# Optimization experiments

Hardware: AMD Instinct MI355X
Metric: run time of the kernel (lower is better)

## Reference

```python
import jax, jax.numpy as jnp
import numpy as np
import math

V, H, NH, L, S, B = 100000, 2048, 64, 2, 512, 2
HD = H // NH  # 32
MAX_LEN = 5000
EPS_NORM = 1e-5
EPS_ATTN = 1e-6


def build_pe():
    # PositionalEncoding buffer: pe[max_len, 1, d_model]
    position = jnp.arange(MAX_LEN, dtype=jnp.float32)[:, None]
    div_term = jnp.exp(jnp.arange(0, H, 2, dtype=jnp.float32) * (-math.log(10000.0) / H))
    ang = position * div_term  # [max_len, H/2]
    pe = jnp.zeros((MAX_LEN, 1, H), dtype=jnp.float32)
    pe = pe.at[:, 0, 0::2].set(jnp.sin(ang))
    pe = pe.at[:, 0, 1::2].set(jnp.cos(ang))
    return pe


def fast_inv_sqrt(x):
    # Quake fast inverse sqrt; the bit-trick seed is detached in the original
    x2 = x * 0.5
    i = jax.lax.bitcast_convert_type(jax.lax.stop_gradient(x.astype(jnp.float32)), jnp.int32)
    i = jnp.int32(1597463007) - (i >> 1)
    y = jax.lax.bitcast_convert_type(i, jnp.float32)
    return y * (1.5 - x2 * y * y)  # grad flows only through x2, as in torch


def sr_norm(h, w, b):
    mean = h.mean(-1, keepdims=True)
    var = ((h - mean) ** 2).mean(-1, keepdims=True)  # biased variance
    inv = fast_inv_sqrt(var + EPS_NORM)
    return w * ((h - mean) * inv) + b


def attn_layer(x, wq, bq, wk, bk, wv, bv, wo, bo, nw, nb):
    # x: [B, S, H]; weights stored [in, out]
    def heads(t):
        return t.reshape(B, S, NH, HD).transpose(0, 2, 1, 3)  # [B, NH, S, HD]
    q = heads(x @ wq + bq)
    k = heads(x @ wk + bk)
    v = heads(x @ wv + bv)
    scores = jnp.einsum('bhqd,bhkd->bhqk', q, k) / math.sqrt(HD)
    a = jax.nn.softmax(scores, axis=-1)
    # dropout is identity in eval; then double softmax (exp/sum) + sigmoid gate
    e = jnp.exp(a)
    a2 = e / (e.sum(-1, keepdims=True) + EPS_ATTN)
    cw = a2 * jax.nn.sigmoid(a2)
    o = jnp.einsum('bhqk,bhkd->bhqd', cw, v)
    o = o.transpose(0, 2, 1, 3).reshape(B, S, H)
    o = o @ wo + bo
    return sr_norm(o + x, nw, nb)


def setup_inputs():
    key = jax.random.key(0)
    ks = jax.random.split(key, 12)
    def rn(k, shape):
        return jax.random.normal(k, shape, dtype=jnp.float32) * 0.02
    return {
        'src': jax.random.randint(ks[0], (B, S), 0, V),
        'emb': jax.random.uniform(ks[1], (V, H), minval=-0.1, maxval=0.1, dtype=jnp.float32),
        'Wq': rn(ks[2], (L, H, H)), 'bq': jnp.zeros((L, H), jnp.float32),
        'Wk': rn(ks[3], (L, H, H)), 'bk': jnp.zeros((L, H), jnp.float32),
        'Wv': rn(ks[4], (L, H, H)), 'bv': jnp.zeros((L, H), jnp.float32),
        'Wo': rn(ks[5], (L, H, H)), 'bo': jnp.zeros((L, H), jnp.float32),
        'nw': jnp.ones((L, H), jnp.float32), 'nb': jnp.zeros((L, H), jnp.float32),
        'Wout': jax.random.uniform(ks[6], (H, V), minval=-0.1, maxval=0.1, dtype=jnp.float32),
        'bout': jnp.zeros((V,), jnp.float32),
    }


def reference(src, emb, Wq, bq, Wk, bk, Wv, bv, Wo, bo, nw, nb, Wout, bout):
    x = emb[src] * math.sqrt(H)  # [B, S, H]
    pe = build_pe()
    # Faithful to pe[:x.size(0)] where x is [B, S, H]: indexes by BATCH dim
    x = x + pe[:x.shape[0]]  # [B, 1, H] broadcast over seq
    for l in range(L):
        x = attn_layer(x, Wq[l], bq[l], Wk[l], bk[l], Wv[l], bv[l],
                       Wo[l], bo[l], nw[l], nb[l])
    return x @ Wout + bout  # [B, S, V]
```

## Files before the change

kernel.cpp:

```cpp
#include <hip/hip_runtime.h>


#define DEVINL __device__ __forceinline__

typedef float f32x4 __attribute__((ext_vector_type(4)));
typedef __bf16 bf16x8 __attribute__((ext_vector_type(8)));

DEVINL unsigned short f2bf(float f) {
  unsigned int u = __float_as_uint(f);
  u += 0x7fffu + ((u >> 16) & 1u);
  return (unsigned short)(u >> 16);
}

DEVINL void gload_lds16(const void* g, void* l) {
  __builtin_amdgcn_global_load_lds(
      (const __attribute__((address_space(1))) unsigned int*)g,
      (__attribute__((address_space(3))) unsigned int*)l, 16, 0, 0);
}

__global__ __launch_bounds__(256) void embed_kernel(
    const int* __restrict__ src, const float* __restrict__ emb,
    float* __restrict__ x, unsigned short* __restrict__ xbf) {
  const int row = blockIdx.x;
  const int b = row >> 9;
  const int tok = src[row];
  const float sqrtH = 45.25483399593904f;
  const float c = -9.210340371976184f / 2048.f;
  for (int h = threadIdx.x; h < 2048; h += 256) {
    int i = h >> 1;
    float dv = expf((float)(2 * i) * c);
    float ang = (float)b * dv;
    float pe = (h & 1) ? cosf(ang) : sinf(ang);
    float val = emb[(size_t)tok * 2048 + h] * sqrtH + pe;
    x[(size_t)row * 2048 + h] = val;
    xbf[(size_t)row * 2048 + h] = f2bf(val);
  }
}

template <int BM>
DEVINL void gemm_body(const unsigned short* __restrict__ A, const float* __restrict__ B,
                      const float* __restrict__ bias, float* __restrict__ C,
                      const int N, const int m0, const int n0) {
  constexpr int K = 2048;
  constexpr int WM = BM / 32;
  constexpr int AI = BM / 64;
  __shared__ __align__(16) unsigned short A_lds[2][BM * 32];
  __shared__ __align__(16) unsigned short B_lds[2][128 * 32];

  const int tid = threadIdx.x;
  const int w = tid >> 6, lane = tid & 63;
  const int wm = w >> 1, wn = w & 1;

  const int n_local = tid & 127;
  const int kq = tid >> 7;
  const int col = n0 + n_local;
  const bool colok = col < N;
  const int bswz = (n_local >> 1) & 3;

  const int aRow = lane >> 2;
  const int aChunk = (lane & 3) ^ ((lane >> 3) & 3);

  int aOff[WM], bOff[4];
#pragma unroll
  for (int mi = 0; mi < WM; ++mi) {
    int m = wm * (BM / 2) + mi * 16 + (lane & 15);
    aOff[mi] = m * 32 + ((lane >> 4) ^ ((m >> 1) & 3)) * 8;
  }
#pragma unroll
  for (int ni = 0; ni < 4; ++ni) {
    int n = wn * 64 + ni * 16 + (lane & 15);
    bOff[ni] = n * 32 + ((lane >> 4) ^ ((n >> 1) & 3)) * 8;
  }

  f32x4 acc[WM][4] = {};
  float fB[16];

  auto stageA = [&](int k0, int bf) {
#pragma unroll
    for (int i = 0; i < AI; ++i) {
      int r0 = (w * AI + i) * 16;
      gload_lds16(A + (size_t)(m0 + r0 + aRow) * K + k0 + aChunk * 8,
                  &A_lds[bf][r0 * 32]);
    }
  };
  auto loadB = [&](int k0) {
#pragma unroll
    for (int g = 0; g < 4; ++g) {
      int kl = (g * 2 + kq) * 4;
#pragma unroll
      for (int i = 0; i < 4; ++i)
        fB[g * 4 + i] = colok ? B[(size_t)(k0 + kl + i) * N + col] : 0.f;
    }
  };
  auto writeB = [&](int bf) {
#pragma unroll
    for (int g = 0; g < 4; ++g) {
      int kl = (g * 2 + kq) * 4;
      unsigned int lo = (unsigned int)f2bf(fB[g * 4 + 0]) | ((unsigned int)f2bf(fB[g * 4 + 1]) << 16);
      unsigned int hi = (unsigned int)f2bf(fB[g * 4 + 2]) | ((unsigned int)f2bf(fB[g * 4 + 3]) << 16);
      int chunk = (kl >> 3) ^ bswz;
      *(uint2*)&B_lds[bf][n_local * 32 + chunk * 8 + (kl & 7)] = make_uint2(lo, hi);
    }
  };
  auto compute = [&](int bf) {
    bf16x8 af[WM], bfr[4];
#pragma unroll
    for (int mi = 0; mi < WM; ++mi) af[mi] = *(const bf16x8*)&A_lds[bf][aOff[mi]];
#pragma unroll
    for (int ni = 0; ni < 4; ++ni) bfr[ni] = *(const bf16x8*)&B_lds[bf][bOff[ni]];
#pragma unroll
    for (int mi = 0; mi < WM; ++mi)
#pragma unroll
      for (int ni = 0; ni < 4; ++ni)
        acc[mi][ni] = __builtin_amdgcn_mfma_f32_16x16x32_bf16(af[mi], bfr[ni], acc[mi][ni], 0, 0, 0);
  };

  stageA(0, 0);
  loadB(0);
  writeB(0);
  __syncthreads();
  int buf = 0;
  for (int t = 0; t < K / 32 - 1; ++t) {
    stageA((t + 1) * 32, buf ^ 1);
    loadB((t + 1) * 32);
    compute(buf);
    writeB(buf ^ 1);
    __syncthreads();
    buf ^= 1;
  }
  compute(buf);

  const int r0w = (lane >> 4) * 4;
  const int lrow = lane & 15;
#pragma unroll
  for (int mi = 0; mi < WM; ++mi)
#pragma unroll
    for (int ni = 0; ni < 4; ++ni) {
      int ccol = n0 + wn * 64 + ni * 16 + lrow;
      if (ccol < N) {
        float bv = bias[ccol];
#pragma unroll
        for (int r = 0; r < 4; ++r) {
          int crow = m0 + wm * (BM / 2) + mi * 16 + r0w + r;
          C[(size_t)crow * N + ccol] = acc[mi][ni][r] + bv;
        }
      }
    }
}

template <int BM>
__global__ __launch_bounds__(256) void gemm_kernel(
    const unsigned short* __restrict__ A, const float* __restrict__ B,
    const float* __restrict__ bias, float* __restrict__ C, const int N) {
  gemm_body<BM>(A, B, bias, C, N, blockIdx.x * BM, blockIdx.y * 128);
}

__global__ __launch_bounds__(256) void gemm_qkv_kernel(
    const unsigned short* __restrict__ A,
    const float* __restrict__ Wq, const float* __restrict__ Wk, const float* __restrict__ Wv,
    const float* __restrict__ bq, const float* __restrict__ bk, const float* __restrict__ bv,
    float* __restrict__ q, float* __restrict__ k, float* __restrict__ v) {
  const int z = blockIdx.z;
  const float* B = (z == 0) ? Wq : (z == 1) ? Wk : Wv;
  const float* bias = (z == 0) ? bq : (z == 1) ? bk : bv;
  float* C = (z == 0) ? q : (z == 1) ? k : v;
  gemm_body<64>(A, B, bias, C, 2048, blockIdx.x * 64, blockIdx.y * 128);
}

__global__ __launch_bounds__(256) void gemm_final_kernel(
    const unsigned short* __restrict__ A, const float* __restrict__ B,
    const float* __restrict__ bias, float* __restrict__ C, const int N) {
  const int bid = blockIdx.x;
  const int f = (bid & 7) * (gridDim.x >> 3) + (bid >> 3);
  gemm_body<128>(A, B, bias, C, N, (f & 7) * 128, (f >> 3) * 128);
}

__global__ __launch_bounds__(256) void attn_kernel(
    const float* __restrict__ q, const float* __restrict__ k,
    const float* __restrict__ v, unsigned short* __restrict__ o) {
  __shared__ __align__(16) float K_lds[512 * 32];
  const int tid = threadIdx.x;
  const int blk = blockIdx.x;
  const int bh = blk >> 1, chunk = blk & 1;
  const int b = bh >> 6, h = bh & 63;
  const size_t headoff = (size_t)b * 512 * 2048 + (size_t)h * 32;

  const float* kb = k + headoff;
#pragma unroll
  for (int i = 0; i < 16; ++i) {
    int flat = i * 256 + tid;
    int j = flat >> 3, d4 = flat & 7;
    *(float4*)&K_lds[j * 32 + d4 * 4] = *(const float4*)(kb + (size_t)j * 2048 + d4 * 4);
  }
  __syncthreads();

  const int row = chunk * 256 + tid;
  const float* qr = q + headoff + (size_t)row * 2048;
  float4 Q[8];
#pragma unroll
  for (int d = 0; d < 8; ++d) Q[d] = *(const float4*)(qr + d * 4);

  const float scale = 0.17677669529663689f;
  auto dot = [&](int j) -> float {
    const float4* kr = (const float4*)&K_lds[j * 32];
    float p0 = 0.f, p1 = 0.f, p2 = 0.f, p3 = 0.f;
#pragma unroll
    for (int d = 0; d < 8; ++d) {
      float4 kk = kr[d];
      p0 = fmaf(Q[d].x, kk.x, p0);
      p1 = fmaf(Q[d].y, kk.y, p1);
      p2 = fmaf(Q[d].z, kk.z, p2);
      p3 = fmaf(Q[d].w, kk.w, p3);
    }
    return ((p0 + p1) + (p2 + p3)) * scale;
  };

  float m = -1e30f, denom = 0.f;
  for (int j = 0; j < 512; ++j) {
    float s = dot(j);
    float nm = fmaxf(m, s);
    denom = denom * __expf(m - nm) + __expf(s - nm);
    m = nm;
  }
  const float invd = 1.f / denom;

  float sum_e = 0.f;
  for (int j = 0; j < 512; ++j) {
    float a = __expf(dot(j) - m) * invd;
    sum_e += __expf(a);
  }
  const float inv_se = 1.f / (sum_e + 1e-6f);

  float4 accv[8];
#pragma unroll
  for (int d = 0; d < 8; ++d) accv[d] = make_float4(0.f, 0.f, 0.f, 0.f);
  const float* vb = v + headoff;
  float4 vcur[8];
#pragma unroll
  for (int d = 0; d < 8; ++d) vcur[d] = ((const float4*)vb)[d];
  for (int j = 0; j < 512; ++j) {
    float4 vnxt[8];
    if (j < 511) {
      const float4* vr = (const float4*)(vb + (size_t)(j + 1) * 2048);
#pragma unroll
      for (int d = 0; d < 8; ++d) vnxt[d] = vr[d];
    } else {
#pragma unroll
      for (int d = 0; d < 8; ++d) vnxt[d] = vcur[d];
    }
    float a = __expf(dot(j) - m) * invd;
    float e = __expf(a);
    float a2 = e * inv_se;
    float cw = a2 / (1.f + __expf(-a2));
#pragma unroll
    for (int d = 0; d < 8; ++d) {
      accv[d].x = fmaf(cw, vcur[d].x, accv[d].x);
      accv[d].y = fmaf(cw, vcur[d].y, accv[d].y);
      accv[d].z = fmaf(cw, vcur[d].z, accv[d].z);
      accv[d].w = fmaf(cw, vcur[d].w, accv[d].w);
    }
#pragma unroll
    for (int d = 0; d < 8; ++d) vcur[d] = vnxt[d];
  }
  unsigned short* orow = o + headoff + (size_t)row * 2048;
#pragma unroll
  for (int d = 0; d < 8; ++d) {
    orow[d * 4 + 0] = f2bf(accv[d].x);
    orow[d * 4 + 1] = f2bf(accv[d].y);
    orow[d * 4 + 2] = f2bf(accv[d].z);
    orow[d * 4 + 3] = f2bf(accv[d].w);
  }
}

__global__ __launch_bounds__(256) void norm_kernel(
    const float* __restrict__ o, const float* __restrict__ xin,
    const float* __restrict__ w, const float* __restrict__ bb,
    float* __restrict__ xout, unsigned short* __restrict__ xbf) {
  __shared__ float red[4];
  const int row = blockIdx.x, tid = threadIdx.x;
  const float* op = o + (size_t)row * 2048;
  const float* xp = xin + (size_t)row * 2048;
  float4 hv[2];
#pragma unroll
  for (int i = 0; i < 2; ++i) {
    float4 a = *(const float4*)(op + tid * 4 + i * 1024);
    float4 c = *(const float4*)(xp + tid * 4 + i * 1024);
    hv[i] = make_float4(a.x + c.x, a.y + c.y, a.z + c.z, a.w + c.w);
  }
  float s = 0.f;
#pragma unroll
  for (int i = 0; i < 2; ++i) s += hv[i].x + hv[i].y + hv[i].z + hv[i].w;
  for (int off = 32; off; off >>= 1) s += __shfl_down(s, off);
  if ((tid & 63) == 0) red[tid >> 6] = s;
  __syncthreads();
  const float mean = (red[0] + red[1] + red[2] + red[3]) * (1.f / 2048.f);
  __syncthreads();

  float vs = 0.f;
#pragma unroll
  for (int i = 0; i < 2; ++i) {
    float dx = hv[i].x - mean, dy = hv[i].y - mean, dz = hv[i].z - mean, dw = hv[i].w - mean;
    vs += dx * dx + dy * dy + dz * dz + dw * dw;
  }
  for (int off = 32; off; off >>= 1) vs += __shfl_down(vs, off);
  if ((tid & 63) == 0) red[tid >> 6] = vs;
  __syncthreads();
  const float var = (red[0] + red[1] + red[2] + red[3]) * (1.f / 2048.f);

  const float xv = var + 1e-5f;
  int ii = __float_as_int(xv);
  ii = 1597463007 - (ii >> 1);
  float y = __int_as_float(ii);
  y = y * (1.5f - 0.5f * xv * y * y);

#pragma unroll
  for (int i = 0; i < 2; ++i) {
    int c0 = tid * 4 + i * 1024;
    float4 wv = *(const float4*)(w + c0);
    float4 bv = *(const float4*)(bb + c0);
    float r0 = wv.x * ((hv[i].x - mean) * y) + bv.x;
    float r1 = wv.y * ((hv[i].y - mean) * y) + bv.y;
    float r2 = wv.z * ((hv[i].z - mean) * y) + bv.z;
    float r3 = wv.w * ((hv[i].w - mean) * y) + bv.w;
    *(float4*)(xout + (size_t)row * 2048 + c0) = make_float4(r0, r1, r2, r3);
    unsigned short* xb = xbf + (size_t)row * 2048 + c0;
    xb[0] = f2bf(r0); xb[1] = f2bf(r1); xb[2] = f2bf(r2); xb[3] = f2bf(r3);
  }
}

extern "C" void kernel_launch(void* const* d_in, const int* in_sizes, int n_in,
                              void* d_out, int out_size, void* d_ws, size_t ws_size,
                              hipStream_t stream) {
  const int*   src  = (const int*)d_in[0];
  const float* emb  = (const float*)d_in[1];
  const float* Wq   = (const float*)d_in[2];
  const float* bq   = (const float*)d_in[3];
  const float* Wk   = (const float*)d_in[4];
  const float* bk   = (const float*)d_in[5];
  const float* Wv   = (const float*)d_in[6];
  const float* bv   = (const float*)d_in[7];
  const float* Wo   = (const float*)d_in[8];
  const float* bo   = (const float*)d_in[9];
  const float* nw   = (const float*)d_in[10];
  const float* nb   = (const float*)d_in[11];
  const float* Wout = (const float*)d_in[12];
  const float* bout = (const float*)d_in[13];
  float* out = (float*)d_out;

  char* ws = (char*)d_ws;
  float* x  = (float*)(ws);
  float* qb = (float*)(ws + (8ll << 20));
  float* kb = (float*)(ws + (16ll << 20));
  float* vb = (float*)(ws + (24ll << 20));
  float* ob = (float*)(ws + (32ll << 20));
  unsigned short* xbf = (unsigned short*)(ws + (40ll << 20));
  unsigned short* abf = (unsigned short*)(ws + (44ll << 20));

  embed_kernel<<<1024, 256, 0, stream>>>(src, emb, x, xbf);

  for (int l = 0; l < 2; ++l) {
    const size_t wo_ = (size_t)l * 2048 * 2048;
    const size_t bo_ = (size_t)l * 2048;
    gemm_qkv_kernel<<<dim3(16, 16, 3), 256, 0, stream>>>(
        xbf, Wq + wo_, Wk + wo_, Wv + wo_, bq + bo_, bk + bo_, bv + bo_, qb, kb, vb);
    attn_kernel<<<256, 256, 0, stream>>>(qb, kb, vb, abf);
    gemm_kernel<64><<<dim3(16, 16), 256, 0, stream>>>(abf, Wo + wo_, bo + bo_, ob, 2048);
    norm_kernel<<<1024, 256, 0, stream>>>(ob, x, nw + bo_, nb + bo_, x, xbf);
  }

  gemm_final_kernel<<<8 * 782, 256, 0, stream>>>(xbf, Wout, bout, out, 100000);
}
```

Before: 2.095 ms.

## Pre-transpose weights to bf16 K-major and load GEMM B tiles directly to LDS

Adds a transpose kernel that converts each fp32 weight matrix into a bf16 [N,K] copy in workspace. GEMMs then stage B tiles with direct global-to-LDS loads instead of strided fp32 loads followed by in-register conversion. The conversion runs every call and rereads the full 800MB Wout while writing a 400MB bf16 copy, so it adds traffic in exchange for cheaper GEMM inner loops. Also switches bf16 packing to native conversions with vectorised stores. It falls back to the old path when the workspace is too small.

```diff
diff --git a/kernel.cpp b/kernel.cpp
--- a/kernel.cpp
+++ b/kernel.cpp
@@ -5,11 +5,18 @@
 
 typedef float f32x4 __attribute__((ext_vector_type(4)));
 typedef __bf16 bf16x8 __attribute__((ext_vector_type(8)));
-
-DEVINL unsigned short f2bf(float f) {
-  unsigned int u = __float_as_uint(f);
-  u += 0x7fffu + ((u >> 16) & 1u);
-  return (unsigned short)(u >> 16);
+typedef __bf16 bf16x2v __attribute__((ext_vector_type(2)));
+
+DEVINL unsigned int pk2(float a, float b) {
+  bf16x2v v;
+  v[0] = (__bf16)a;
+  v[1] = (__bf16)b;
+  return __builtin_bit_cast(unsigned int, v);
+}
+
+DEVINL unsigned short bf1(float a) {
+  __bf16 v = (__bf16)a;
+  return __builtin_bit_cast(unsigned short, v);
 }
 
 DEVINL void gload_lds16(const void* g, void* l) {
@@ -33,8 +40,140 @@
     float pe = (h & 1) ? cosf(ang) : sinf(ang);
     float val = emb[(size_t)tok * 2048 + h] * sqrtH + pe;
     x[(size_t)row * 2048 + h] = val;
-    xbf[(size_t)row * 2048 + h] = f2bf(val);
-  }
+    xbf[(size_t)row * 2048 + h] = bf1(val);
+  }
+}
+
+__global__ __launch_bounds__(256) void wtrans_kernel(
+    const float* __restrict__ W, unsigned short* __restrict__ WT, const int N) {
+  __shared__ float t[64][65];
+  const int tid = threadIdx.x;
+  const int n0 = blockIdx.x * 64, k0 = blockIdx.y * 64;
+#pragma unroll
+  for (int i = 0; i < 16; ++i) {
+    int kl = i * 4 + (tid >> 6);
+    int n = n0 + (tid & 63);
+    t[kl][tid & 63] = (n < N) ? W[(size_t)(k0 + kl) * N + n] : 0.f;
+  }
+  __syncthreads();
+#pragma unroll
+  for (int j = 0; j < 8; ++j) {
+    int nl = j * 8 + (tid >> 5);
+    int kp = (tid & 31) * 2;
+    unsigned int u = pk2(t[kp][nl], t[kp + 1][nl]);
+    *(unsigned int*)&WT[(size_t)(n0 + nl) * 2048 + k0 + kp] = u;
+  }
+}
+
+template <int BM, int NN>
+DEVINL void gemm_bf_body(const unsigned short* __restrict__ A,
+                         const unsigned short* __restrict__ BT,
+                         const float* __restrict__ bias, float* __restrict__ C,
+                         const int m0, const int n0) {
+  constexpr int K = 2048;
+  constexpr int WM = BM / 32;
+  __shared__ __align__(16) unsigned short A_lds[2][BM * 32];
+  __shared__ __align__(16) unsigned short B_lds[2][128 * 32];
+
+  const int tid = threadIdx.x;
+  const int w = tid >> 6, lane = tid & 63;
+  const int wm = w >> 1, wn = w & 1;
+
+  const int aRow = lane >> 2;
+  const int aChunk = (lane & 3) ^ ((lane >> 3) & 3);
+
+  int aOff[WM], bOff[4];
+#pragma unroll
+  for (int mi = 0; mi < WM; ++mi) {
+    int m = wm * (BM / 2) + mi * 16 + (lane & 15);
+    aOff[mi] = m * 32 + ((lane >> 4) ^ ((m >> 1) & 3)) * 8;
+  }
+#pragma unroll
+  for (int ni = 0; ni < 4; ++ni) {
+    int n = wn * 64 + ni * 16 + (lane & 15);
+    bOff[ni] = n * 32 + ((lane >> 4) ^ ((n >> 1) & 3)) * 8;
+  }
+
+  f32x4 acc[WM][4] = {};
+
+  auto stage = [&](int k0, int bf) {
+#pragma unroll
+    for (int i = 0; i < BM / 64; ++i) {
+      int r0 = (w * (BM / 64) + i) * 16;
+      gload_lds16(A + (size_t)(m0 + r0 + aRow) * K + k0 + aChunk * 8, &A_lds[bf][r0 * 32]);
+    }
+#pragma unroll
+    for (int i = 0; i < 2; ++i) {
+      int r0 = (w * 2 + i) * 16;
+      gload_lds16(BT + (size_t)(n0 + r0 + aRow) * K + k0 + aChunk * 8, &B_lds[bf][r0 * 32]);
+    }
+  };
+  auto compute = [&](int bf) {
+    bf16x8 af[WM], bfr[4];
+#pragma unroll
+    for (int mi = 0; mi < WM; ++mi) af[mi] = *(const bf16x8*)&A_lds[bf][aOff[mi]];
+#pragma unroll
+    for (int ni = 0; ni < 4; ++ni) bfr[ni] = *(const bf16x8*)&B_lds[bf][bOff[ni]];
+#pragma unroll
+    for (int mi = 0; mi < WM; ++mi)
+#pragma unroll
+      for (int ni = 0; ni < 4; ++ni)
+        acc[mi][ni] = __builtin_amdgcn_mfma_f32_16x16x32_bf16(af[mi], bfr[ni], acc[mi][ni], 0, 0, 0);
+  };
+
+  stage(0, 0);
+  __syncthreads();
+  int buf = 0;
+  for (int t = 0; t < K / 32 - 1; ++t) {
+    stage((t + 1) * 32, buf ^ 1);
+    compute(buf);
+    __syncthreads();
+    buf ^= 1;
+  }
+  compute(buf);
+
+  const int r0w = (lane >> 4) * 4;
+  const int lrow = lane & 15;
+#pragma unroll
+  for (int mi = 0; mi < WM; ++mi)
+#pragma unroll
+    for (int ni = 0; ni < 4; ++ni) {
+      int ccol = n0 + wn * 64 + ni * 16 + lrow;
+      if ((NN % 128 == 0) || ccol < NN) {
+        float bv = bias[ccol];
+#pragma unroll
+        for (int r = 0; r < 4; ++r) {
+          int crow = m0 + wm * (BM / 2) + mi * 16 + r0w + r;
+          C[(size_t)crow * NN + ccol] = acc[mi][ni][r] + bv;
+        }
+      }
+    }
+}
+
+template <int BM, int NN>
+__global__ __launch_bounds__(256) void gemm_bf_kernel(
+    const unsigned short* __restrict__ A, const unsigned short* __restrict__ BT,
+    const float* __restrict__ bias, float* __restrict__ C) {
+  gemm_bf_body<BM, NN>(A, BT, bias, C, blockIdx.x * BM, blockIdx.y * 128);
+}
+
+__global__ __launch_bounds__(256) void gemm_qkv_bf_kernel(
+    const unsigned short* __restrict__ A, const unsigned short* __restrict__ WT,
+    const float* __restrict__ bq, const float* __restrict__ bk, const float* __restrict__ bv,
+    float* __restrict__ q, float* __restrict__ k, float* __restrict__ v) {
+  const int z = blockIdx.z;
+  const unsigned short* BT = WT + (size_t)z * 2048 * 2048;
+  const float* bias = (z == 0) ? bq : (z == 1) ? bk : bv;
+  float* C = (z == 0) ? q : (z == 1) ? k : v;
+  gemm_bf_body<64, 2048>(A, BT, bias, C, blockIdx.x * 64, blockIdx.y * 128);
+}
+
+__global__ __launch_bounds__(256) void gemm_final_bf_kernel(
+    const unsigned short* __restrict__ A, const unsigned short* __restrict__ BT,
+    const float* __restrict__ bias, float* __restrict__ C) {
+  const int bid = blockIdx.x;
+  const int f = (bid & 7) * (gridDim.x >> 3) + (bid >> 3);
+  gemm_bf_body<128, 100000>(A, BT, bias, C, (f & 7) * 128, (f >> 3) * 128);
 }
 
 template <int BM>
@@ -79,8 +218,7 @@
 #pragma unroll
     for (int i = 0; i < AI; ++i) {
       int r0 = (w * AI + i) * 16;
-      gload_lds16(A + (size_t)(m0 + r0 + aRow) * K + k0 + aChunk * 8,
-                  &A_lds[bf][r0 * 32]);
+      gload_lds16(A + (size_t)(m0 + r0 + aRow) * K + k0 + aChunk * 8, &A_lds[bf][r0 * 32]);
     }
   };
   auto loadB = [&](int k0) {
@@ -96,10 +234,10 @@
 #pragma unroll
     for (int g = 0; g < 4; ++g) {
       int kl = (g * 2 + kq) * 4;
-      unsigned int lo = (unsigned int)f2bf(fB[g * 4 + 0]) | ((unsigned int)f2bf(fB[g * 4 + 1]) << 16);
-      unsigned int hi = (unsigned int)f2bf(fB[g * 4 + 2]) | ((unsigned int)f2bf(fB[g * 4 + 3]) << 16);
+      uint2 p = make_uint2(pk2(fB[g * 4 + 0], fB[g * 4 + 1]),
+                           pk2(fB[g * 4 + 2], fB[g * 4 + 3]));
       int chunk = (kl >> 3) ^ bswz;
-      *(uint2*)&B_lds[bf][n_local * 32 + chunk * 8 + (kl & 7)] = make_uint2(lo, hi);
+      *(uint2*)&B_lds[bf][n_local * 32 + chunk * 8 + (kl & 7)] = p;
     }
   };
   auto compute = [&](int bf) {
@@ -146,13 +284,6 @@
         }
       }
     }
-}
-
-template <int BM>
-__global__ __launch_bounds__(256) void gemm_kernel(
-    const unsigned short* __restrict__ A, const float* __restrict__ B,
-    const float* __restrict__ bias, float* __restrict__ C, const int N) {
-  gemm_body<BM>(A, B, bias, C, N, blockIdx.x * BM, blockIdx.y * 128);
 }
 
 __global__ __launch_bounds__(256) void gemm_qkv_kernel(
@@ -167,6 +298,13 @@
   gemm_body<64>(A, B, bias, C, 2048, blockIdx.x * 64, blockIdx.y * 128);
 }
 
+template <int BM>
+__global__ __launch_bounds__(256) void gemm_kernel(
+    const unsigned short* __restrict__ A, const float* __restrict__ B,
+    const float* __restrict__ bias, float* __restrict__ C, const int N) {
+  gemm_body<BM>(A, B, bias, C, N, blockIdx.x * BM, blockIdx.y * 128);
+}
+
 __global__ __launch_bounds__(256) void gemm_final_kernel(
     const unsigned short* __restrict__ A, const float* __restrict__ B,
     const float* __restrict__ bias, float* __restrict__ C, const int N) {
@@ -265,10 +403,8 @@
   unsigned short* orow = o + headoff + (size_t)row * 2048;
 #pragma unroll
   for (int d = 0; d < 8; ++d) {
-    orow[d * 4 + 0] = f2bf(accv[d].x);
-    orow[d * 4 + 1] = f2bf(accv[d].y);
-    orow[d * 4 + 2] = f2bf(accv[d].z);
-    orow[d * 4 + 3] = f2bf(accv[d].w);
+    uint2 p = make_uint2(pk2(accv[d].x, accv[d].y), pk2(accv[d].z, accv[d].w));
+    *(uint2*)&orow[d * 4] = p;
   }
 }
 
@@ -323,8 +459,7 @@
     float r2 = wv.z * ((hv[i].z - mean) * y) + bv.z;
     float r3 = wv.w * ((hv[i].w - mean) * y) + bv.w;
     *(float4*)(xout + (size_t)row * 2048 + c0) = make_float4(r0, r1, r2, r3);
-    unsigned short* xb = xbf + (size_t)row * 2048 + c0;
-    xb[0] = f2bf(r0); xb[1] = f2bf(r1); xb[2] = f2bf(r2); xb[3] = f2bf(r3);
+    *(uint2*)&xbf[(size_t)row * 2048 + c0] = make_uint2(pk2(r0, r1), pk2(r2, r3));
   }
 }
 
@@ -356,17 +491,44 @@
   unsigned short* xbf = (unsigned short*)(ws + (40ll << 20));
   unsigned short* abf = (unsigned short*)(ws + (44ll << 20));
 
+  const unsigned long long NEED = (112ull << 20) + 100096ull * 2048ull * 2ull;
+  const bool big = (unsigned long long)ws_size >= NEED;
+  unsigned short* WTp = (unsigned short*)(ws + (48ll << 20));
+  unsigned short* WTo = (unsigned short*)(ws + (112ll << 20));
+
   embed_kernel<<<1024, 256, 0, stream>>>(src, emb, x, xbf);
 
-  for (int l = 0; l < 2; ++l) {
-    const size_t wo_ = (size_t)l * 2048 * 2048;
-    const size_t bo_ = (size_t)l * 2048;
-    gemm_qkv_kernel<<<dim3(16, 16, 3), 256, 0, stream>>>(
-        xbf, Wq + wo_, Wk + wo_, Wv + wo_, bq + bo_, bk + bo_, bv + bo_, qb, kb, vb);
-    attn_kernel<<<256, 256, 0, stream>>>(qb, kb, vb, abf);
-    gemm_kernel<64><<<dim3(16, 16), 256, 0, stream>>>(abf, Wo + wo_, bo + bo_, ob, 2048);
-    norm_kernel<<<1024, 256, 0, stream>>>(ob, x, nw + bo_, nb + bo_, x, xbf);
-  }
-
-  gemm_final_kernel<<<8 * 782, 256, 0, stream>>>(xbf, Wout, bout, out, 100000);
-}
+  if (big) {
+    for (int l = 0; l < 2; ++l) {
+      const size_t wo_ = (size_t)l * 2048 * 2048;
+      const float* Wm[4] = {Wq + wo_, Wk + wo_, Wv + wo_, Wo + wo_};
+      for (int mt = 0; mt < 4; ++mt)
+        wtrans_kernel<<<dim3(32, 32), 256, 0, stream>>>(
+            Wm[mt], WTp + (size_t)(l * 4 + mt) * 2048 * 2048, 2048);
+    }
+    wtrans_kernel<<<dim3(1564, 32), 256, 0, stream>>>(Wout, WTo, 100000);
+
+    for (int l = 0; l < 2; ++l) {
+      const size_t bo_ = (size_t)l * 2048;
+      const unsigned short* WTl = WTp + (size_t)(l * 4) * 2048 * 2048;
+      gemm_qkv_bf_kernel<<<dim3(16, 16, 3), 256, 0, stream>>>(
+          xbf, WTl, bq + bo_, bk + bo_, bv + bo_, qb, kb, vb);
+      attn_kernel<<<256, 256, 0, stream>>>(qb, kb, vb, abf);
+      gemm_bf_kernel<64, 2048><<<dim3(16, 16), 256, 0, stream>>>(
+          abf, WTl + (size_t)3 * 2048 * 2048, bo + bo_, ob);
+      norm_kernel<<<1024, 256, 0, stream>>>(ob, x, nw + bo_, nb + bo_, x, xbf);
+    }
+    gemm_final_bf_kernel<<<8 * 782, 256, 0, stream>>>(xbf, WTo, bout, out);
+  } else {
+    for (int l = 0; l < 2; ++l) {
+      const size_t wo_ = (size_t)l * 2048 * 2048;
+      const size_t bo_ = (size_t)l * 2048;
+      gemm_qkv_kernel<<<dim3(16, 16, 3), 256, 0, stream>>>(
+          xbf, Wq + wo_, Wk + wo_, Wv + wo_, bq + bo_, bk + bo_, bv + bo_, qb, kb, vb);
+      attn_kernel<<<256, 256, 0, stream>>>(qb, kb, vb, abf);
+      gemm_kernel<64><<<dim3(16, 16), 256, 0, stream>>>(abf, Wo + wo_, bo + bo_, ob, 2048);
+      norm_kernel<<<1024, 256, 0, stream>>>(ob, x, nw + bo_, nb + bo_, x, xbf);
+    }
+    gemm_final_kernel<<<8 * 782, 256, 0, stream>>>(xbf, Wout, bout, out, 100000);
+  }
+}
```

Measured after the change: 1.962 ms. 1.07x faster.
